# Kernel tuning notes

Measured on AMD Instinct MI355X. Metric: run time of the kernel, lower is better.

Reference implementation:

```python
import jax, jax.numpy as jnp
import numpy as np

N, TD, TE, D = 8, 1024, 2048, 1024

def setup_inputs() -> dict:
    key = jax.random.key(0)
    kq, km, kl = jax.random.split(key, 3)
    queries = jax.random.normal(kq, (N, TD, D), dtype=jnp.float32)
    memory = jax.random.normal(km, (N, TE, D), dtype=jnp.float32)
    # lengths in [1, TE] so no row is fully masked (avoids NaN softmax)
    lengths = jax.random.randint(kl, (N,), 1, TE + 1, dtype=jnp.int32)
    return {"queries": queries, "memory": memory, "lengths": lengths}

def reference(queries, memory, lengths):
    scale = jnp.asarray(np.sqrt(D), dtype=queries.dtype)
    # [N, Td, Te] = bmm(queries, memory^T) / sqrt(D)
    weights = jnp.einsum('ntd,nsd->nts', queries, memory) / scale
    # padding mask: position s is invalid if s >= lengths[n]
    mask = jnp.arange(TE)[None, :] >= lengths[:, None]          # [N, Te]
    weights = jnp.where(mask[:, None, :], -jnp.inf, weights)
    alignments = jax.nn.softmax(weights, axis=-1)               # [N, Td, Te]
    contexts = jnp.einsum('nts,nsd->ntd', alignments, memory)   # [N, Td, D]
    return (contexts, alignments)
```

## Files before the change

### kernel.cpp

```cpp
#include <hip/hip_runtime.h>
#include <hip/hip_bf16.h>

#define NB 8
#define TDIM 1024
#define TEDIM 2048
#define DDIM 1024

typedef __bf16 bf16x8 __attribute__((ext_vector_type(8)));
typedef float f32x4 __attribute__((ext_vector_type(4)));
typedef unsigned short us8 __attribute__((ext_vector_type(8)));

static __device__ __forceinline__ void gld_lds16(const __bf16* g, __bf16* l) {
    __builtin_amdgcn_global_load_lds(
        (const __attribute__((address_space(1))) void*)g,
        (__attribute__((address_space(3))) void*)l,
        16, 0, 0);
}

static __device__ __forceinline__ unsigned short bf16_bits(float f) {
    __bf16 h = (__bf16)f;
    return __builtin_bit_cast(unsigned short, h);
}
static __device__ __forceinline__ float bits_f32(unsigned short u) {
    return (float)__builtin_bit_cast(__bf16, u);
}

__global__ __launch_bounds__(256) void prepass_kernel(
    const float* __restrict__ Q, const float* __restrict__ M,
    __bf16* __restrict__ Qb, __bf16* __restrict__ Mb, __bf16* __restrict__ Mt,
    const int* __restrict__ len_p)
{
    const int z = blockIdx.z;
    const int t = threadIdx.x;

    if (z >= NB) {
        const int flat = (z - NB) * 512 + blockIdx.y * 32 + blockIdx.x;
        const size_t base = (size_t)flat * 8192 + (size_t)t * 8;
        #pragma unroll
        for (int c = 0; c < 4; ++c) {
            const size_t i = base + (size_t)c * 2048;
            float4 a = *reinterpret_cast<const float4*>(&Q[i]);
            float4 b = *reinterpret_cast<const float4*>(&Q[i + 4]);
            us8 o;
            o[0] = bf16_bits(a.x); o[1] = bf16_bits(a.y);
            o[2] = bf16_bits(a.z); o[3] = bf16_bits(a.w);
            o[4] = bf16_bits(b.x); o[5] = bf16_bits(b.y);
            o[6] = bf16_bits(b.z); o[7] = bf16_bits(b.w);
            *reinterpret_cast<us8*>(&Qb[i]) = o;
        }
        return;
    }

    const int n  = z;
    const int s0 = blockIdx.x * 64;
    if (s0 >= len_p[n]) return;
    const int d0 = blockIdx.y * 64;
    const float* Mn  = M  + (size_t)n * TEDIM * DDIM;
    __bf16*      Mbn = Mb + (size_t)n * TEDIM * DDIM;
    __bf16*      Mtn = Mt + (size_t)n * DDIM * TEDIM;

    __shared__ float tile[64][65];

    #pragma unroll
    for (int j = 0; j < 4; ++j) {
        const int flat = j * 256 + t;
        const int r  = flat >> 4;
        const int c4 = (flat & 15) * 4;
        float4 v = *reinterpret_cast<const float4*>(
            &Mn[(size_t)(s0 + r) * DDIM + d0 + c4]);
        tile[r][c4 + 0] = v.x; tile[r][c4 + 1] = v.y;
        tile[r][c4 + 2] = v.z; tile[r][c4 + 3] = v.w;
        ushort4 o;
        o.x = bf16_bits(v.x); o.y = bf16_bits(v.y);
        o.z = bf16_bits(v.z); o.w = bf16_bits(v.w);
        *reinterpret_cast<ushort4*>(&Mbn[(size_t)(s0 + r) * DDIM + d0 + c4]) = o;
    }
    __syncthreads();

    const int dr  = t >> 2;
    const int sc0 = (t & 3) * 16;
    us8 o0, o1;
    #pragma unroll
    for (int i = 0; i < 8; ++i)  o0[i] = bf16_bits(tile[sc0 + i][dr]);
    #pragma unroll
    for (int i = 0; i < 8; ++i)  o1[i] = bf16_bits(tile[sc0 + 8 + i][dr]);
    __bf16* dst = &Mtn[(size_t)(d0 + dr) * TEDIM + s0 + sc0];
    *reinterpret_cast<us8*>(dst)     = o0;
    *reinterpret_cast<us8*>(dst + 8) = o1;
}

template<int LDA, int LDB, int LDC, int KDIM, long SA, long SB, long SC,
         bool COLPAIR, bool SCALE, bool OUTBF16, bool KBOUND>
__global__ __launch_bounds__(256) void gemm_kernel(
    const __bf16* __restrict__ A, const __bf16* __restrict__ B,
    void* __restrict__ Cv, const int* __restrict__ len_p)
{
    const int n   = blockIdx.z;
    const int len = len_p[n];
    int ct;
    if constexpr (COLPAIR) {
        const int xc = blockIdx.x;
        ct = (xc < 8) ? xc : 23 - xc;
        if (ct * 128 >= len) return;
    } else {
        ct = blockIdx.x;
    }
    const int col0 = ct * 128;
    const int row0 = blockIdx.y * 128;
    const int klim = KBOUND ? ((len + 63) & ~63) : KDIM;

    const __bf16* Ab = A + (size_t)n * SA + (size_t)row0 * LDA;
    const __bf16* Bb = B + (size_t)n * SB + (size_t)col0 * LDB;

    __shared__ __align__(16) __bf16 As[128 * 64];
    __shared__ __align__(16) __bf16 Bs[128 * 64];

    const int t    = threadIdx.x;
    const int lane = t & 63;
    const int w    = t >> 6;
    const int wr   = (w >> 1) * 64;
    const int wc   = (w & 1) * 64;

    f32x4 acc[4][4] = {};

    for (int k0 = 0; k0 < klim; k0 += 64) {
        #pragma unroll
        for (int j = 0; j < 4; ++j) {
            const int slot = j * 256 + t;
            const int r    = slot >> 3;
            const int cg   = (slot & 7) ^ (r & 7);
            gld_lds16(Ab + (size_t)r * LDA + k0 + cg * 8, &As[slot * 8]);
            gld_lds16(Bb + (size_t)r * LDB + k0 + cg * 8, &Bs[slot * 8]);
        }
        __syncthreads();

        bf16x8 af[2][4], bfr[2][4];
        #pragma unroll
        for (int kk = 0; kk < 2; ++kk) {
            #pragma unroll
            for (int i = 0; i < 4; ++i) {
                const int rowa = wr + i * 16 + (lane & 15);
                const int ca   = (kk * 4 + (lane >> 4)) ^ (rowa & 7);
                af[kk][i] = *reinterpret_cast<const bf16x8*>(
                    &As[rowa * 64 + ca * 8]);
                const int rowb = wc + i * 16 + (lane & 15);
                const int cb   = (kk * 4 + (lane >> 4)) ^ (rowb & 7);
                bfr[kk][i] = *reinterpret_cast<const bf16x8*>(
                    &Bs[rowb * 64 + cb * 8]);
            }
        }

        #pragma unroll
        for (int kk = 0; kk < 2; ++kk)
            #pragma unroll
            for (int i = 0; i < 4; ++i)
                #pragma unroll
                for (int j = 0; j < 4; ++j)
                    acc[i][j] = __builtin_amdgcn_mfma_f32_16x16x32_bf16(
                        af[kk][i], bfr[kk][j], acc[i][j], 0, 0, 0);
        __syncthreads();
    }

    const float sc = SCALE ? 0.03125f : 1.0f;
    #pragma unroll
    for (int i = 0; i < 4; ++i) {
        #pragma unroll
        for (int j = 0; j < 4; ++j) {
            const int col   = col0 + wc + j * 16 + (lane & 15);
            const int rbase = row0 + wr + i * 16 + (lane >> 4) * 4;
            #pragma unroll
            for (int r = 0; r < 4; ++r) {
                const size_t idx = (size_t)n * SC + (size_t)(rbase + r) * LDC + col;
                if constexpr (OUTBF16)
                    ((__bf16*)Cv)[idx] = (__bf16)(acc[i][j][r] * sc);
                else
                    ((float*)Cv)[idx] = acc[i][j][r] * sc;
            }
        }
    }
}

__global__ __launch_bounds__(256) void softmax_kernel(
    __bf16* __restrict__ P, float* __restrict__ Sout,
    const int* __restrict__ len_p)
{
    const int row = blockIdx.x;
    const int n   = row >> 10;
    const int len = len_p[n];
    const int kmax = (len + 63) & ~63;
    __bf16* Pr = P    + (size_t)row * TEDIM;
    float*  Sr = Sout + (size_t)row * TEDIM;

    const int t    = threadIdx.x;
    const int lane = t & 63;
    const int w    = t >> 6;
    const int s0   = t * 8;

    float v[8];
    if (s0 < len) {
        us8 raw = *reinterpret_cast<const us8*>(&Pr[s0]);
        #pragma unroll
        for (int i = 0; i < 8; ++i) {
            v[i] = bits_f32(raw[i]);
            if (s0 + i >= len) v[i] = -INFINITY;
        }
    } else {
        #pragma unroll
        for (int i = 0; i < 8; ++i) v[i] = -INFINITY;
    }

    float mx = v[0];
    #pragma unroll
    for (int i = 1; i < 8; ++i) mx = fmaxf(mx, v[i]);
    #pragma unroll
    for (int off = 32; off; off >>= 1) mx = fmaxf(mx, __shfl_xor(mx, off));

    __shared__ float redm[4], reds[4];
    if (lane == 0) redm[w] = mx;
    __syncthreads();
    mx = fmaxf(fmaxf(redm[0], redm[1]), fmaxf(redm[2], redm[3]));

    float e[8];
    float sum = 0.f;
    #pragma unroll
    for (int i = 0; i < 8; ++i) { e[i] = __expf(v[i] - mx); sum += e[i]; }
    #pragma unroll
    for (int off = 32; off; off >>= 1) sum += __shfl_xor(sum, off);
    if (lane == 0) reds[w] = sum;
    __syncthreads();
    sum = reds[0] + reds[1] + reds[2] + reds[3];

    const float r = 1.0f / sum;
    float p[8];
    #pragma unroll
    for (int i = 0; i < 8; ++i) p[i] = e[i] * r;

    float4 oa = {p[0], p[1], p[2], p[3]};
    float4 ob = {p[4], p[5], p[6], p[7]};
    *reinterpret_cast<float4*>(&Sr[s0])     = oa;
    *reinterpret_cast<float4*>(&Sr[s0 + 4]) = ob;

    if (s0 < kmax) {
        us8 o;
        #pragma unroll
        for (int i = 0; i < 8; ++i) o[i] = bf16_bits(p[i]);
        *reinterpret_cast<us8*>(&Pr[s0]) = o;
    }
}

extern "C" void kernel_launch(void* const* d_in, const int* in_sizes, int n_in,
                              void* d_out, int out_size, void* d_ws, size_t ws_size,
                              hipStream_t stream) {
    const float* Q       = (const float*)d_in[0];
    const float* M       = (const float*)d_in[1];
    const int*   lengths = (const int*)d_in[2];

    float* ctx   = (float*)d_out;
    float* align = ctx + (size_t)NB * TDIM * DDIM;

    __bf16* Qb = (__bf16*)d_ws;
    __bf16* Mb = Qb + (size_t)NB * TDIM * DDIM;
    __bf16* Mt = Mb + (size_t)NB * TEDIM * DDIM;
    __bf16* Pb = Mt + (size_t)NB * DDIM * TEDIM;

    dim3 blk(256);
    prepass_kernel<<<dim3(32, 16, 10), blk, 0, stream>>>(Q, M, Qb, Mb, Mt, lengths);
    gemm_kernel<DDIM, DDIM, TEDIM, DDIM,
                (long)TDIM * DDIM, (long)TEDIM * DDIM, (long)TDIM * TEDIM,
                true, true, true, false>
        <<<dim3(16, TDIM / 128, NB), blk, 0, stream>>>(Qb, Mb, (void*)Pb, lengths);
    softmax_kernel<<<dim3(NB * TDIM), blk, 0, stream>>>(Pb, align, lengths);
    gemm_kernel<TEDIM, TEDIM, DDIM, TEDIM,
                (long)TDIM * TEDIM, (long)DDIM * TEDIM, (long)TDIM * DDIM,
                false, false, false, true>
        <<<dim3(DDIM / 128, TDIM / 128, NB), blk, 0, stream>>>(Pb, Mt, (void*)ctx, lengths);
}
```

Measured before the change: 273.1 us.

## Double-buffer LDS in GEMMs and pair column tiles per score block

```diff
diff --git a/kernel.cpp b/kernel.cpp
--- a/kernel.cpp
+++ b/kernel.cpp
@@ -89,31 +89,77 @@
     *reinterpret_cast<us8*>(dst + 8) = o1;
 }
 
-template<int LDA, int LDB, int LDC, int KDIM, long SA, long SB, long SC,
-         bool COLPAIR, bool SCALE, bool OUTBF16, bool KBOUND>
-__global__ __launch_bounds__(256) void gemm_kernel(
-    const __bf16* __restrict__ A, const __bf16* __restrict__ B,
-    void* __restrict__ Cv, const int* __restrict__ len_p)
-{
-    const int n   = blockIdx.z;
-    const int len = len_p[n];
-    int ct;
-    if constexpr (COLPAIR) {
-        const int xc = blockIdx.x;
-        ct = (xc < 8) ? xc : 23 - xc;
-        if (ct * 128 >= len) return;
-    } else {
-        ct = blockIdx.x;
-    }
-    const int col0 = ct * 128;
+template<int LDA, int LDB>
+static __device__ __forceinline__ void tile_gemm_dbuf(
+    const __bf16* __restrict__ Ab, const __bf16* __restrict__ Bb,
+    __bf16* As, __bf16* Bs, int klim, int t, int lane, int wr, int wc,
+    f32x4 (&acc)[4][4])
+{
+    const int nk = klim >> 6;
+
+    auto stage = [&](int buf, int k0) {
+        #pragma unroll
+        for (int j = 0; j < 4; ++j) {
+            const int slot = j * 256 + t;
+            const int r    = slot >> 3;
+            const int cg   = (slot & 7) ^ (r & 7);
+            gld_lds16(Ab + (size_t)r * LDA + k0 + cg * 8,
+                      As + buf * 8192 + slot * 8);
+            gld_lds16(Bb + (size_t)r * LDB + k0 + cg * 8,
+                      Bs + buf * 8192 + slot * 8);
+        }
+    };
+
+    stage(0, 0);
+    int buf = 0;
+    for (int ki = 0; ki < nk; ++ki) {
+        if (ki + 1 < nk) {
+            stage(buf ^ 1, (ki + 1) << 6);
+            asm volatile("s_waitcnt vmcnt(8)" ::: "memory");
+        } else {
+            asm volatile("s_waitcnt vmcnt(0)" ::: "memory");
+        }
+        __builtin_amdgcn_sched_barrier(0);
+        __builtin_amdgcn_s_barrier();
+
+        const __bf16* Ac = As + buf * 8192;
+        const __bf16* Bc = Bs + buf * 8192;
+        #pragma unroll
+        for (int kk = 0; kk < 2; ++kk) {
+            bf16x8 af[4], bfr[4];
+            #pragma unroll
+            for (int i = 0; i < 4; ++i) {
+                const int rowa = wr + i * 16 + (lane & 15);
+                const int ca   = (kk * 4 + (lane >> 4)) ^ (rowa & 7);
+                af[i] = *reinterpret_cast<const bf16x8*>(&Ac[rowa * 64 + ca * 8]);
+                const int rowb = wc + i * 16 + (lane & 15);
+                const int cb   = (kk * 4 + (lane >> 4)) ^ (rowb & 7);
+                bfr[i] = *reinterpret_cast<const bf16x8*>(&Bc[rowb * 64 + cb * 8]);
+            }
+            #pragma unroll
+            for (int i = 0; i < 4; ++i)
+                #pragma unroll
+                for (int j = 0; j < 4; ++j)
+                    acc[i][j] = __builtin_amdgcn_mfma_f32_16x16x32_bf16(
+                        af[i], bfr[j], acc[i][j], 0, 0, 0);
+        }
+        asm volatile("s_waitcnt lgkmcnt(0)" ::: "memory");
+        __builtin_amdgcn_sched_barrier(0);
+        __builtin_amdgcn_s_barrier();
+        buf ^= 1;
+    }
+}
+
+__global__ __launch_bounds__(256) void scores_kernel(
+    const __bf16* __restrict__ Qb, const __bf16* __restrict__ Mb,
+    __bf16* __restrict__ Pb, const int* __restrict__ len_p)
+{
+    const int n    = blockIdx.z;
+    const int len  = len_p[n];
     const int row0 = blockIdx.y * 128;
-    const int klim = KBOUND ? ((len + 63) & ~63) : KDIM;
-
-    const __bf16* Ab = A + (size_t)n * SA + (size_t)row0 * LDA;
-    const __bf16* Bb = B + (size_t)n * SB + (size_t)col0 * LDB;
-
-    __shared__ __align__(16) __bf16 As[128 * 64];
-    __shared__ __align__(16) __bf16 Bs[128 * 64];
+
+    __shared__ __align__(16) __bf16 As[2 * 128 * 64];
+    __shared__ __align__(16) __bf16 Bs[2 * 128 * 64];
 
     const int t    = threadIdx.x;
     const int lane = t & 63;
@@ -121,47 +167,61 @@
     const int wr   = (w >> 1) * 64;
     const int wc   = (w & 1) * 64;
 
+    const __bf16* Ab = Qb + (size_t)n * TDIM * DDIM + (size_t)row0 * DDIM;
+    __bf16*       Cb = Pb + (size_t)n * TDIM * TEDIM;
+
+    const int cts[2] = {(int)blockIdx.x, 15 - (int)blockIdx.x};
+    #pragma unroll
+    for (int p = 0; p < 2; ++p) {
+        const int ct   = cts[p];
+        const int col0 = ct * 128;
+        if (col0 >= len) continue;
+
+        const __bf16* Bb = Mb + (size_t)n * TEDIM * DDIM + (size_t)col0 * DDIM;
+        f32x4 acc[4][4] = {};
+        tile_gemm_dbuf<DDIM, DDIM>(Ab, Bb, As, Bs, DDIM, t, lane, wr, wc, acc);
+
+        #pragma unroll
+        for (int i = 0; i < 4; ++i) {
+            #pragma unroll
+            for (int j = 0; j < 4; ++j) {
+                const int col   = col0 + wc + j * 16 + (lane & 15);
+                const int rbase = row0 + wr + i * 16 + (lane >> 4) * 4;
+                #pragma unroll
+                for (int r = 0; r < 4; ++r)
+                    Cb[(size_t)(rbase + r) * TEDIM + col] =
+                        (__bf16)(acc[i][j][r] * 0.03125f);
+            }
+        }
+    }
+}
+
+__global__ __launch_bounds__(256) void contexts_kernel(
+    const __bf16* __restrict__ Pb, const __bf16* __restrict__ Mt,
+    float* __restrict__ C, const int* __restrict__ len_p)
+{
+    const int n    = blockIdx.z;
+    const int len  = len_p[n];
+    const int klim = (len + 63) & ~63;
+    const int col0 = blockIdx.x * 128;
+    const int row0 = blockIdx.y * 128;
+
+    __shared__ __align__(16) __bf16 As[2 * 128 * 64];
+    __shared__ __align__(16) __bf16 Bs[2 * 128 * 64];
+
+    const int t    = threadIdx.x;
+    const int lane = t & 63;
+    const int w    = t >> 6;
+    const int wr   = (w >> 1) * 64;
+    const int wc   = (w & 1) * 64;
+
+    const __bf16* Ab = Pb + (size_t)n * TDIM * TEDIM + (size_t)row0 * TEDIM;
+    const __bf16* Bb = Mt + (size_t)n * DDIM * TEDIM + (size_t)col0 * TEDIM;
+    float*        Cb = C  + (size_t)n * TDIM * DDIM;
+
     f32x4 acc[4][4] = {};
-
-    for (int k0 = 0; k0 < klim; k0 += 64) {
-        #pragma unroll
-        for (int j = 0; j < 4; ++j) {
-            const int slot = j * 256 + t;
-            const int r    = slot >> 3;
-            const int cg   = (slot & 7) ^ (r & 7);
-            gld_lds16(Ab + (size_t)r * LDA + k0 + cg * 8, &As[slot * 8]);
-            gld_lds16(Bb + (size_t)r * LDB + k0 + cg * 8, &Bs[slot * 8]);
-        }
-        __syncthreads();
-
-        bf16x8 af[2][4], bfr[2][4];
-        #pragma unroll
-        for (int kk = 0; kk < 2; ++kk) {
-            #pragma unroll
-            for (int i = 0; i < 4; ++i) {
-                const int rowa = wr + i * 16 + (lane & 15);
-                const int ca   = (kk * 4 + (lane >> 4)) ^ (rowa & 7);
-                af[kk][i] = *reinterpret_cast<const bf16x8*>(
-                    &As[rowa * 64 + ca * 8]);
-                const int rowb = wc + i * 16 + (lane & 15);
-                const int cb   = (kk * 4 + (lane >> 4)) ^ (rowb & 7);
-                bfr[kk][i] = *reinterpret_cast<const bf16x8*>(
-                    &Bs[rowb * 64 + cb * 8]);
-            }
-        }
-
-        #pragma unroll
-        for (int kk = 0; kk < 2; ++kk)
-            #pragma unroll
-            for (int i = 0; i < 4; ++i)
-                #pragma unroll
-                for (int j = 0; j < 4; ++j)
-                    acc[i][j] = __builtin_amdgcn_mfma_f32_16x16x32_bf16(
-                        af[kk][i], bfr[kk][j], acc[i][j], 0, 0, 0);
-        __syncthreads();
-    }
-
-    const float sc = SCALE ? 0.03125f : 1.0f;
+    tile_gemm_dbuf<TEDIM, TEDIM>(Ab, Bb, As, Bs, klim, t, lane, wr, wc, acc);
+
     #pragma unroll
     for (int i = 0; i < 4; ++i) {
         #pragma unroll
@@ -169,13 +229,8 @@
             const int col   = col0 + wc + j * 16 + (lane & 15);
             const int rbase = row0 + wr + i * 16 + (lane >> 4) * 4;
             #pragma unroll
-            for (int r = 0; r < 4; ++r) {
-                const size_t idx = (size_t)n * SC + (size_t)(rbase + r) * LDC + col;
-                if constexpr (OUTBF16)
-                    ((__bf16*)Cv)[idx] = (__bf16)(acc[i][j][r] * sc);
-                else
-                    ((float*)Cv)[idx] = acc[i][j][r] * sc;
-            }
+            for (int r = 0; r < 4; ++r)
+                Cb[(size_t)(rbase + r) * DDIM + col] = acc[i][j][r];
         }
     }
 }
@@ -265,13 +320,8 @@
 
     dim3 blk(256);
     prepass_kernel<<<dim3(32, 16, 10), blk, 0, stream>>>(Q, M, Qb, Mb, Mt, lengths);
-    gemm_kernel<DDIM, DDIM, TEDIM, DDIM,
-                (long)TDIM * DDIM, (long)TEDIM * DDIM, (long)TDIM * TEDIM,
-                true, true, true, false>
-        <<<dim3(16, TDIM / 128, NB), blk, 0, stream>>>(Qb, Mb, (void*)Pb, lengths);
+    scores_kernel<<<dim3(8, TDIM / 128, NB), blk, 0, stream>>>(Qb, Mb, Pb, lengths);
     softmax_kernel<<<dim3(NB * TDIM), blk, 0, stream>>>(Pb, align, lengths);
-    gemm_kernel<TEDIM, TEDIM, DDIM, TEDIM,
-                (long)TDIM * TEDIM, (long)DDIM * TEDIM, (long)TDIM * DDIM,
-                false, false, false, true>
-        <<<dim3(DDIM / 128, TDIM / 128, NB), blk, 0, stream>>>(Pb, Mt, (void*)ctx, lengths);
-}
+    contexts_kernel<<<dim3(DDIM / 128, TDIM / 128, NB), blk, 0, stream>>>(
+        Pb, Mt, ctx, lengths);
+}
```

Result: faster. 266.9 us (-2.3%).
